# Kernel optimization log

Hardware: AMD Instinct MI355X
Metric: run time of the kernel (lower is better)

## Reference

```python
import jax, jax.numpy as jnp
import numpy as np

W_DIM, B_DIM, S = 8, 8, 900  # patches: [W, B, 1, 30, 30] -> seq_len 900


def setup_inputs() -> dict:
    key = jax.random.key(0)
    ks = jax.random.split(key, 8)
    radar = jax.random.normal(ks[0], (W_DIM, B_DIM, 1, 30, 30), jnp.float32)
    dmde = jax.random.normal(ks[1], (W_DIM, B_DIM, 1, 30, 30), jnp.float32)
    gumbel_u = jax.random.uniform(ks[2], (B_DIM * W_DIM, S, S), jnp.float32)
    # MHA with embed_dim=1 -> all projections are scalars (xavier-ish init)
    Wq = jax.random.normal(ks[3], (), jnp.float32)
    Wk = jax.random.normal(ks[4], (), jnp.float32)
    Wv = jax.random.normal(ks[5], (), jnp.float32)
    Wo = jax.random.normal(ks[6], (), jnp.float32)
    bq = jnp.zeros((), jnp.float32)
    bk = jnp.zeros((), jnp.float32)
    bv = jnp.zeros((), jnp.float32)
    bo = jnp.zeros((), jnp.float32)
    ln_gamma = jnp.ones((), jnp.float32)
    ln_beta = jnp.zeros((), jnp.float32)
    attn_residual_scale = jnp.asarray(1e-9, jnp.float32)
    return dict(radar_patches=radar, dmde_out_patches=dmde, gumbel_u=gumbel_u,
                Wq=Wq, bq=bq, Wk=Wk, bk=bk, Wv=Wv, bv=bv, Wo=Wo, bo=bo,
                ln_gamma=ln_gamma, ln_beta=ln_beta,
                attn_residual_scale=attn_residual_scale)


def reference(radar_patches, dmde_out_patches, gumbel_u, Wq, bq, Wk, bk, Wv, bv,
              Wo, bo, ln_gamma, ln_beta, attn_residual_scale):
    Wd, B = radar_patches.shape[0], radar_patches.shape[1]
    # [W,B,1,30,30] -> [B*W, S]
    radar = jnp.transpose(radar_patches, (1, 0, 2, 3, 4)).reshape(B * Wd, -1)
    mde = jnp.transpose(dmde_out_patches, (1, 0, 2, 3, 4)).reshape(B * Wd, -1)
    # --- cross attention, embed_dim = head_dim = 1 (scale = 1/sqrt(1) = 1) ---
    q = radar * Wq + bq
    k = mde * Wk + bk
    v = mde * Wv + bv
    attn = jax.nn.softmax(jnp.einsum('ni,nj->nij', q, k), axis=-1)  # [N,S,S]
    attended = jnp.einsum('nij,nj->ni', attn, v) * Wo + bo           # [N,S]
    # LayerNorm over last dim of size 1 (degenerate: output == ln_beta)
    x = (radar + attended)[..., None]                                # [N,S,1]
    mu = jnp.mean(x, axis=-1, keepdims=True)
    var = jnp.mean((x - mu) ** 2, axis=-1, keepdims=True)
    attended_out = (x - mu) / jnp.sqrt(var + 1e-5) * ln_gamma + ln_beta
    # --- hard gumbel attention gather/scatter, fully mask-vectorized ---
    valid = (radar != 0).astype(radar.dtype)                          # [N,S]
    noise = -jnp.log(-jnp.log(gumbel_u + 1e-8) + 1e-8)
    p = jax.nn.softmax(attn + noise, axis=-1)  # temperature = 1.0
    idx = jnp.argmax(p, axis=-1)                                      # [N,S]
    y_hard = jax.nn.one_hot(idx, p.shape[-1], dtype=p.dtype)
    y = jax.lax.stop_gradient(y_hard - p) + p                         # straight-through
    src = radar * valid   # invalid rows contribute nothing (matches per-row loop)
    out_seq = jnp.einsum('nts,nt->ns', y, src)[..., None]             # [N,S,1]
    combined = valid[..., None] * (out_seq != 0).astype(out_seq.dtype)
    out_seq = out_seq + combined * (attn_residual_scale * attended_out)
    # [N,S] -> [B,W,S] -> [B,1,S,W]
    out = out_seq[..., 0].reshape(B, Wd, -1).transpose(0, 2, 1)[:, None]
    return out
```

## Files before the change

### kernel.cpp

```cpp
#include <hip/hip_runtime.h>
#include <cfloat>

#define SS 900
#define WD 8
#define BD 8
#define NROWS 64
#define OUT_ELEMS (BD * SS * WD)
#define NQ 225
#define KPAD 904

__global__ __launch_bounds__(256) void rel_prep(
    const float* __restrict__ mde,
    const float* __restrict__ pWk, const float* __restrict__ pbk,
    float* __restrict__ kws,
    float* __restrict__ kext,
    float* __restrict__ out)
{
    const int tid = threadIdx.x;
    const int n   = blockIdx.x;

    for (int i = n * 256 + tid; i < OUT_ELEMS; i += 64 * 256) out[i] = 0.0f;

    const float wk = pWk[0], bk0 = pbk[0];
    const int b = n >> 3, w = n & 7;
    const float* __restrict__ mrow = mde + (size_t)(w * BD + b) * SS;

    float kmin = FLT_MAX, kmax = -FLT_MAX;
    #pragma unroll
    for (int j = 0; j < 4; j++) {
        int s = j * 256 + tid;
        if (s < SS) {
            float k = __fmaf_rn(mrow[s], wk, bk0);
            kws[(size_t)n * KPAD + s] = k;
            kmin = fminf(kmin, k);
            kmax = fmaxf(kmax, k);
        }
    }
    #pragma unroll
    for (int off = 1; off < 64; off <<= 1) {
        kmin = fminf(kmin, __shfl_xor(kmin, off, 64));
        kmax = fmaxf(kmax, __shfl_xor(kmax, off, 64));
    }
    __shared__ float s_min[4], s_max[4];
    if ((tid & 63) == 0) { s_min[tid >> 6] = kmin; s_max[tid >> 6] = kmax; }
    __syncthreads();
    if (tid == 0) {
        kext[2 * n]     = fminf(fminf(s_min[0], s_min[1]), fminf(s_min[2], s_min[3]));
        kext[2 * n + 1] = fmaxf(fmaxf(s_max[0], s_max[1]), fmaxf(s_max[2], s_max[3]));
    }
}

__global__ __launch_bounds__(256) void rel_main(
    const float* __restrict__ radar,
    const float* __restrict__ gumbel,
    const float* __restrict__ kws,
    const float* __restrict__ kext,
    const float* __restrict__ pWq, const float* __restrict__ pbq,
    float* __restrict__ out)
{
    const int wid  = threadIdx.x >> 6;
    const int lane = threadIdx.x & 63;
    const int row  = blockIdx.x * 4 + wid;
    const int n    = row / SS;
    const int t    = row - n * SS;
    const int b    = n >> 3;
    const int w    = n & 7;

    const float4* __restrict__ g4 = (const float4*)(gumbel + (size_t)row * SS);
    const float4* __restrict__ k4 = (const float4*)(kws + (size_t)n * KPAD);
    const float*  __restrict__ rrow = radar + (size_t)(w * BD + b) * SS;

    const float q = __fmaf_rn(rrow[t], pWq[0], pbq[0]);
    const float kmin = kext[2 * n], kmax = kext[2 * n + 1];
    const float m = __fmul_rn(q, (q >= 0.0f) ? kmax : kmin);

    float4 U[4], K[4];
    float umax = -1.0f;
    float D = 0.0f;
    #pragma unroll
    for (int j = 0; j < 4; j++) {
        int f = j * 64 + lane;
        bool valid = (f < NQ);
        int fc = valid ? f : 0;
        float4 u = g4[fc];
        float4 k = k4[fc];
        K[j] = k;
        if (!valid) { u.x = u.y = u.z = u.w = -1.0f; }
        U[j] = u;
        umax = fmaxf(umax, fmaxf(fmaxf(u.x, u.y), fmaxf(u.z, u.w)));
        if (valid) {
            D += __expf(__fmaf_rn(q, k.x, -m)) + __expf(__fmaf_rn(q, k.y, -m))
               + __expf(__fmaf_rn(q, k.z, -m)) + __expf(__fmaf_rn(q, k.w, -m));
        }
    }
    #pragma unroll
    for (int off = 1; off < 64; off <<= 1) {
        umax = fmaxf(umax, __shfl_xor(umax, off, 64));
        D += __shfl_xor(D, off, 64);
    }

    float w0    = -logf(umax + 1e-8f);
    float nzmax = -logf(w0 + 1e-8f);
    float T     = nzmax - 1.05f;
    float wT    = expf(-T);
    float uthr  = expf(-(wT - 1e-8f)) - 1e-8f;
    uthr = uthr - fabsf(uthr) * 4e-6f - 1e-9f;

    float bestv = -FLT_MAX;
    int   besti = 0x7fffffff;
    #pragma unroll
    for (int j = 0; j < 4; j++) {
        int f = j * 64 + lane;
        float4 u = U[j];
        float4 k = K[j];
        int s0 = f * 4;
        if (u.x >= uthr) {
            float l = __fmul_rn(q, k.x);
            float nz = -logf(-logf(u.x + 1e-8f) + 1e-8f);
            float v = expf(l - m) / D + nz;
            if (v > bestv) { bestv = v; besti = s0; }
        }
        if (u.y >= uthr) {
            float l = __fmul_rn(q, k.y);
            float nz = -logf(-logf(u.y + 1e-8f) + 1e-8f);
            float v = expf(l - m) / D + nz;
            if (v > bestv) { bestv = v; besti = s0 + 1; }
        }
        if (u.z >= uthr) {
            float l = __fmul_rn(q, k.z);
            float nz = -logf(-logf(u.z + 1e-8f) + 1e-8f);
            float v = expf(l - m) / D + nz;
            if (v > bestv) { bestv = v; besti = s0 + 2; }
        }
        if (u.w >= uthr) {
            float l = __fmul_rn(q, k.w);
            float nz = -logf(-logf(u.w + 1e-8f) + 1e-8f);
            float v = expf(l - m) / D + nz;
            if (v > bestv) { bestv = v; besti = s0 + 3; }
        }
    }
    #pragma unroll
    for (int off = 1; off < 64; off <<= 1) {
        float ov = __shfl_xor(bestv, off, 64);
        int   oi = __shfl_xor(besti, off, 64);
        if (ov > bestv || (ov == bestv && oi < besti)) { bestv = ov; besti = oi; }
    }
    if (lane == 0)
        atomicAdd(&out[((size_t)b * SS + besti) * WD + w], rrow[t]);
}

__global__ __launch_bounds__(256) void rel_epilogue(
    const float* __restrict__ radar,
    const float* __restrict__ pScale,
    const float* __restrict__ pBeta,
    float* __restrict__ out)
{
    int i = blockIdx.x * 256 + threadIdx.x;
    if (i >= OUT_ELEMS) return;
    int w    = i & 7;
    int rest = i >> 3;
    int s    = rest % SS;
    int b    = rest / SS;
    float o = out[i];
    float r = radar[(size_t)(w * BD + b) * SS + s];
    float add = ((r != 0.0f) && (o != 0.0f)) ? (pScale[0] * pBeta[0]) : 0.0f;
    out[i] = o + add;
}

extern "C" void kernel_launch(void* const* d_in, const int* in_sizes, int n_in,
                              void* d_out, int out_size, void* d_ws, size_t ws_size,
                              hipStream_t stream) {
    const float* radar  = (const float*)d_in[0];
    const float* mde    = (const float*)d_in[1];
    const float* gumbel = (const float*)d_in[2];
    const float* Wq     = (const float*)d_in[3];
    const float* bq     = (const float*)d_in[4];
    const float* Wk     = (const float*)d_in[5];
    const float* bk     = (const float*)d_in[6];
    const float* beta   = (const float*)d_in[12];
    const float* scale  = (const float*)d_in[13];
    float* out = (float*)d_out;

    float* kws  = (float*)d_ws;
    float* kext = kws + (size_t)NROWS * KPAD;

    rel_prep<<<NROWS, 256, 0, stream>>>(mde, Wk, bk, kws, kext, out);
    rel_main<<<(NROWS * SS) / 4, 256, 0, stream>>>(radar, gumbel, kws, kext, Wq, bq, out);
    rel_epilogue<<<(OUT_ELEMS + 255) / 256, 256, 0, stream>>>(radar, scale, beta, out);
}
```

Before: 51.15 us.

## Process each attention row with 16 lanes and tighten gumbel pruning threshold

```diff
diff --git a/kernel.cpp b/kernel.cpp
--- a/kernel.cpp
+++ b/kernel.cpp
@@ -58,33 +58,35 @@
     const float* __restrict__ pWq, const float* __restrict__ pbq,
     float* __restrict__ out)
 {
-    const int wid  = threadIdx.x >> 6;
-    const int lane = threadIdx.x & 63;
-    const int row  = blockIdx.x * 4 + wid;
-    const int n    = row / SS;
-    const int t    = row - n * SS;
-    const int b    = n >> 3;
-    const int w    = n & 7;
+    const int tid    = threadIdx.x;
+    const int wid    = tid >> 6;
+    const int g      = (tid >> 4) & 3;
+    const int lane16 = tid & 15;
+    const int row    = blockIdx.x * 16 + wid * 4 + g;
+    const int n      = row / SS;
+    const int t      = row - n * SS;
+    const int b      = n >> 3;
+    const int w      = n & 7;
 
     const float4* __restrict__ g4 = (const float4*)(gumbel + (size_t)row * SS);
     const float4* __restrict__ k4 = (const float4*)(kws + (size_t)n * KPAD);
-    const float*  __restrict__ rrow = radar + (size_t)(w * BD + b) * SS;
+    const float*  __restrict__ krow = kws + (size_t)n * KPAD;
 
-    const float q = __fmaf_rn(rrow[t], pWq[0], pbq[0]);
+    const float r0 = radar[(size_t)(w * BD + b) * SS + t];
+    const float q  = __fmaf_rn(r0, pWq[0], pbq[0]);
     const float kmin = kext[2 * n], kmax = kext[2 * n + 1];
     const float m = __fmul_rn(q, (q >= 0.0f) ? kmax : kmin);
 
-    float4 U[4], K[4];
+    float4 U[15];
     float umax = -1.0f;
     float D = 0.0f;
     #pragma unroll
-    for (int j = 0; j < 4; j++) {
-        int f = j * 64 + lane;
-        bool valid = (f < NQ);
-        int fc = valid ? f : 0;
+    for (int j = 0; j < 15; j++) {
+        const int f = j * 16 + lane16;
+        const bool valid = (j < 14) || (lane16 == 0);
+        const int fc = valid ? f : 0;
         float4 u = g4[fc];
         float4 k = k4[fc];
-        K[j] = k;
         if (!valid) { u.x = u.y = u.z = u.w = -1.0f; }
         U[j] = u;
         umax = fmaxf(umax, fmaxf(fmaxf(u.x, u.y), fmaxf(u.z, u.w)));
@@ -94,14 +96,15 @@
         }
     }
     #pragma unroll
-    for (int off = 1; off < 64; off <<= 1) {
-        umax = fmaxf(umax, __shfl_xor(umax, off, 64));
-        D += __shfl_xor(D, off, 64);
+    for (int off = 1; off < 16; off <<= 1) {
+        umax = fmaxf(umax, __shfl_xor(umax, off, 16));
+        D += __shfl_xor(D, off, 16);
     }
 
+    float margin = __fmaf_rn(1.002f, 1.0f / D, 1e-6f);
     float w0    = -logf(umax + 1e-8f);
     float nzmax = -logf(w0 + 1e-8f);
-    float T     = nzmax - 1.05f;
+    float T     = nzmax - margin;
     float wT    = expf(-T);
     float uthr  = expf(-(wT - 1e-8f)) - 1e-8f;
     uthr = uthr - fabsf(uthr) * 4e-6f - 1e-9f;
@@ -109,44 +112,45 @@
     float bestv = -FLT_MAX;
     int   besti = 0x7fffffff;
     #pragma unroll
-    for (int j = 0; j < 4; j++) {
-        int f = j * 64 + lane;
+    for (int j = 0; j < 15; j++) {
         float4 u = U[j];
-        float4 k = K[j];
-        int s0 = f * 4;
-        if (u.x >= uthr) {
-            float l = __fmul_rn(q, k.x);
-            float nz = -logf(-logf(u.x + 1e-8f) + 1e-8f);
-            float v = expf(l - m) / D + nz;
-            if (v > bestv) { bestv = v; besti = s0; }
-        }
-        if (u.y >= uthr) {
-            float l = __fmul_rn(q, k.y);
-            float nz = -logf(-logf(u.y + 1e-8f) + 1e-8f);
-            float v = expf(l - m) / D + nz;
-            if (v > bestv) { bestv = v; besti = s0 + 1; }
-        }
-        if (u.z >= uthr) {
-            float l = __fmul_rn(q, k.z);
-            float nz = -logf(-logf(u.z + 1e-8f) + 1e-8f);
-            float v = expf(l - m) / D + nz;
-            if (v > bestv) { bestv = v; besti = s0 + 2; }
-        }
-        if (u.w >= uthr) {
-            float l = __fmul_rn(q, k.w);
-            float nz = -logf(-logf(u.w + 1e-8f) + 1e-8f);
-            float v = expf(l - m) / D + nz;
-            if (v > bestv) { bestv = v; besti = s0 + 3; }
+        float m4 = fmaxf(fmaxf(u.x, u.y), fmaxf(u.z, u.w));
+        if (__any(m4 >= uthr)) {
+            const int s0 = (j * 16 + lane16) * 4;
+            if (u.x >= uthr) {
+                float l = __fmul_rn(q, krow[s0]);
+                float nz = -logf(-logf(u.x + 1e-8f) + 1e-8f);
+                float v = expf(l - m) / D + nz;
+                if (v > bestv) { bestv = v; besti = s0; }
+            }
+            if (u.y >= uthr) {
+                float l = __fmul_rn(q, krow[s0 + 1]);
+                float nz = -logf(-logf(u.y + 1e-8f) + 1e-8f);
+                float v = expf(l - m) / D + nz;
+                if (v > bestv) { bestv = v; besti = s0 + 1; }
+            }
+            if (u.z >= uthr) {
+                float l = __fmul_rn(q, krow[s0 + 2]);
+                float nz = -logf(-logf(u.z + 1e-8f) + 1e-8f);
+                float v = expf(l - m) / D + nz;
+                if (v > bestv) { bestv = v; besti = s0 + 2; }
+            }
+            if (u.w >= uthr) {
+                float l = __fmul_rn(q, krow[s0 + 3]);
+                float nz = -logf(-logf(u.w + 1e-8f) + 1e-8f);
+                float v = expf(l - m) / D + nz;
+                if (v > bestv) { bestv = v; besti = s0 + 3; }
+            }
         }
     }
     #pragma unroll
-    for (int off = 1; off < 64; off <<= 1) {
-        float ov = __shfl_xor(bestv, off, 64);
-        int   oi = __shfl_xor(besti, off, 64);
+    for (int off = 1; off < 16; off <<= 1) {
+        float ov = __shfl_xor(bestv, off, 16);
+        int   oi = __shfl_xor(besti, off, 16);
         if (ov > bestv || (ov == bestv && oi < besti)) { bestv = ov; besti = oi; }
     }
-    if (lane == 0)
-        atomicAdd(&out[((size_t)b * SS + besti) * WD + w], rrow[t]);
+    if (lane16 == 0)
+        atomicAdd(&out[((size_t)b * SS + besti) * WD + w], r0);
 }
 
 __global__ __launch_bounds__(256) void rel_epilogue(
@@ -185,6 +189,6 @@
     float* kext = kws + (size_t)NROWS * KPAD;
 
     rel_prep<<<NROWS, 256, 0, stream>>>(mde, Wk, bk, kws, kext, out);
-    rel_main<<<(NROWS * SS) / 4, 256, 0, stream>>>(radar, gumbel, kws, kext, Wq, bq, out);
+    rel_main<<<(NROWS * SS) / 16, 256, 0, stream>>>(radar, gumbel, kws, kext, Wq, bq, out);
     rel_epilogue<<<(OUT_ELEMS + 255) / 256, 256, 0, stream>>>(radar, scale, beta, out);
 }
```

Result: faster. 46.43 us (-9.2%).
